# Kernel optimization log

Hardware: AMD Instinct MI355X
Metric: run time of the kernel (lower is better)

The kernel has to match this reference:

```python
import jax, jax.numpy as jnp
import numpy as np
from jax import lax

B, L, DM = 1, 2048, 1024   # batch, seq len, d_model
N = 16                     # d_state
K = 4                      # d_conv
DI = 2 * DM                # d_inner = d_model * expand_factor


def silu(v):
    return v * jax.nn.sigmoid(v)


def setup_inputs() -> dict:
    key = jax.random.key(0)
    ks = jax.random.split(key, 11)
    s = 0.02
    f32 = jnp.float32
    return {
        "x": jax.random.normal(ks[0], (B, L, DM), f32),
        "W_in": jax.random.normal(ks[1], (2 * DI, DM), f32) * s,
        "b_in": jnp.zeros((2 * DI,), f32),
        "W_conv": jax.random.normal(ks[2], (DI, 1, K), f32) * s,  # depthwise conv kernel (torch layout)
        "b_conv": jnp.zeros((DI,), f32),
        "W_x": jax.random.normal(ks[3], (DI + 2 * N, DI), f32) * s,
        "b_x": jnp.zeros((DI + 2 * N,), f32),
        "W_out": jax.random.normal(ks[4], (DM, DI), f32) * s,
        "b_out": jnp.zeros((DM,), f32),
        "A_log": jax.random.normal(ks[5], (DI, N), f32),
        "D": jnp.ones((DI,), f32),
    }


def reference(x, W_in, b_in, W_conv, b_conv, W_x, b_x, W_out, b_out, A_log, D):
    Bsz = x.shape[0]
    # in_proj and split into ssm branch / residual gate branch
    xr = x @ W_in.T + b_in                      # (B, L, 2*DI)
    xi, res = jnp.split(xr, 2, axis=-1)
    # causal depthwise conv1d: torch pads (K-1) both sides then slices [:L] == left-pad K-1
    xc = jnp.transpose(xi, (0, 2, 1))           # (B, DI, L)
    xc = lax.conv_general_dilated(
        xc, W_conv, window_strides=(1,), padding=[(K - 1, 0)],
        dimension_numbers=("NCH", "OIH", "NCH"), feature_group_count=DI,
    ) + b_conv[None, :, None]
    xi = silu(jnp.transpose(xc, (0, 2, 1)))     # (B, L, DI)
    # selective-scan parameterization
    proj = xi @ W_x.T + b_x                      # (B, L, DI + 2N)
    delta = jax.nn.softplus(proj[..., :DI])      # (B, L, DI)
    B_ssm = proj[..., DI:DI + N]                 # (B, L, N)
    C_ssm = proj[..., DI + N:]                   # (B, L, N)
    A = -jnp.exp(A_log)                          # (DI, N)
    dA = jnp.exp(delta[..., None] * A)                               # (B, L, DI, N)
    dBx = delta[..., None] * B_ssm[:, :, None, :] * xi[..., None]    # (B, L, DI, N)

    def step(h, inp):
        da, dbx, c = inp
        h = da * h + dbx                         # (B, DI, N)
        y = jnp.einsum("bdn,bn->bd", h, c)
        return h, y

    h0 = jnp.zeros((Bsz, DI, N), x.dtype)
    _, ys = lax.scan(
        step, h0,
        (jnp.swapaxes(dA, 0, 1), jnp.swapaxes(dBx, 0, 1), jnp.swapaxes(C_ssm, 0, 1)),
    )
    y = jnp.swapaxes(ys, 0, 1) + xi * D          # skip connection
    y = y * silu(res)                            # gate
    return y @ W_out.T + b_out                   # (B, L, DM)
```

## Files before the change

### kernel.cpp

```cpp
#include <hip/hip_runtime.h>
#include <stdint.h>

#define L_SEQ 2048
#define DMODEL 1024
#define DI_DIM 2048
#define NSSM 16
#define NPROJ 2080
#define NCHUNK 64
#define LCHUNK 32
#define NBC 32

typedef __attribute__((ext_vector_type(8))) short bf16x8;
typedef __attribute__((ext_vector_type(8))) unsigned short u16x8;
typedef __attribute__((ext_vector_type(4))) float f32x4;

__device__ __forceinline__ float bf2f(unsigned short u) {
  union { uint32_t u; float f; } v; v.u = (uint32_t)u << 16; return v.f;
}
__device__ __forceinline__ unsigned short f2bf(float f) {
  union { float f; uint32_t u; } v; v.f = f;
  uint32_t u = v.u;
  return (unsigned short)((u + 0x7fffu + ((u >> 16) & 1u)) >> 16);
}
__device__ __forceinline__ void async16(const void* g, void* l) {
  __builtin_amdgcn_global_load_lds(
      (__attribute__((address_space(1))) void*)(g),
      (__attribute__((address_space(3))) void*)(l), 16, 0, 0);
}
__device__ __forceinline__ float softplusf(float p) {
  return (p > 20.f) ? p : __logf(1.f + __expf(p));
}
__device__ __forceinline__ float siluf(float x) {
  return x * __builtin_amdgcn_rcpf(1.f + __expf(-x));
}

#define WAITV(N) asm volatile("s_waitcnt vmcnt(" #N ")" ::: "memory")
#define GBAR()                                   \
  {                                              \
    __builtin_amdgcn_s_barrier();                \
    asm volatile("" ::: "memory");               \
  }

#define CVT_N1 524288
#define CVT_N2 (CVT_N1 + 1048576)
#define CVT_N3 (CVT_N2 + 1064960)
#define CVT_N4 (CVT_N3 + 524288)
__global__ void k_convert4(const float* __restrict__ x, const float* __restrict__ win,
                           const float* __restrict__ wx, const float* __restrict__ wout,
                           unsigned short* __restrict__ xb, unsigned short* __restrict__ winb,
                           unsigned short* __restrict__ wxb, unsigned short* __restrict__ woutb,
                           unsigned short* __restrict__ wbct) {
  int i = blockIdx.x * 256 + threadIdx.x;
  const float4* src; unsigned short* dst; int j;
  bool isWx = false;
  if (i < CVT_N1)      { src = (const float4*)x;    dst = xb;    j = i; }
  else if (i < CVT_N2) { src = (const float4*)win;  dst = winb;  j = i - CVT_N1; }
  else if (i < CVT_N3) { src = (const float4*)wx;   dst = wxb;   j = i - CVT_N2; isWx = true; }
  else if (i < CVT_N4) { src = (const float4*)wout; dst = woutb; j = i - CVT_N3; }
  else return;
  float4 v = src[j];
  ushort4 o;
  o.x = f2bf(v.x); o.y = f2bf(v.y); o.z = f2bf(v.z); o.w = f2bf(v.w);
  ((ushort4*)dst)[j] = o;
  if (isWx) {
    int r = j >> 9;
    if (r >= DI_DIM) {
      int n = r - DI_DIM;
      int d4 = (j & 511) * 4;
      unsigned short ov[4] = {o.x, o.y, o.z, o.w};
#pragma unroll
      for (int k = 0; k < 4; k++) {
        int d = d4 + k;
        wbct[((size_t)(d >> 3) * NBC + n) * 8 + (d & 7)] = ov[k];
      }
    }
  }
}

__global__ void k_wout_cvt(const float* __restrict__ in, unsigned short* __restrict__ out) {
  int i = blockIdx.x * 256 + threadIdx.x;
  float4 v = ((const float4*)in)[i];
  ushort4 o;
  o.x = f2bf(v.x); o.y = f2bf(v.y); o.z = f2bf(v.z); o.w = f2bf(v.w);
  ((ushort4*)out)[i] = o;
}


#define GSTAGE(BUF, KT)                                                        \
  {                                                                            \
    async16(ap + (KT), &As[BUF][soA]);                                         \
    async16(bp0 + (KT), &Bs[BUF][soB0]);                                       \
    async16(bp1 + (KT), &Bs[BUF][soB1]);                                       \
  }

#define GCOMPUTE(BUF)                                                          \
  {                                                                            \
    bf16x8 af[4], bfv[2];                                                      \
    _Pragma("unroll")                                                          \
    for (int i = 0; i < 4; i++)                                                \
      af[i] = *(const bf16x8*)&As[BUF][i * 512 + ro];                          \
    _Pragma("unroll")                                                          \
    for (int j = 0; j < 2; j++)                                                \
      bfv[j] = *(const bf16x8*)&Bs[BUF][(wave * 2 + j) * 512 + ro];            \
    _Pragma("unroll")                                                          \
    for (int i = 0; i < 4; i++)                                                \
      _Pragma("unroll")                                                        \
      for (int j = 0; j < 2; j++)                                              \
        acc[i][j] = __builtin_amdgcn_mfma_f32_16x16x32_bf16(af[i], bfv[j],     \
                                                        acc[i][j], 0, 0, 0);   \
  }

#define DEFINE_GEMM_BT(NAME, OutT)                                             \
__global__ __launch_bounds__(256) void NAME(                                   \
    const unsigned short* __restrict__ A, const unsigned short* __restrict__ B,\
    const float* __restrict__ bias, OutT* __restrict__ C,                      \
    int M, int N, int K, int ldc) {                                            \
  __shared__ unsigned short As[3][64 * 32];                                    \
  __shared__ unsigned short Bs[3][128 * 32];                                   \
  const int tid = threadIdx.x;                                                 \
  const int wave = tid >> 6;                                                   \
  const int lane = tid & 63;                                                   \
  const int m0 = blockIdx.x * 64;       \
  const int n0 = blockIdx.y * 128;                                             \
  const int kLen = K / gridDim.z;                                              \
  const int kLo = blockIdx.z * kLen;                                           \
  const int srow = lane >> 2;                                                  \
  const int scol = ((lane & 3) ^ ((lane >> 3) & 3)) * 8;                       \
  int ar = m0 + wave * 16 + srow;         if (ar > M - 1) ar = M - 1;          \
  int br0 = n0 + wave * 32 + srow;        if (br0 > N - 1) br0 = N - 1;        \
  int br1 = n0 + wave * 32 + 16 + srow;   if (br1 > N - 1) br1 = N - 1;        \
  const unsigned short* ap  = A + (size_t)ar * K + scol + kLo;                 \
  const unsigned short* bp0 = B + (size_t)br0 * K + scol + kLo;                \
  const unsigned short* bp1 = B + (size_t)br1 * K + scol + kLo;                \
  const int soA  = wave * 512;                                                 \
  const int soB0 = (wave * 2) * 512;                                           \
  const int soB1 = (wave * 2 + 1) * 512;                                       \
  const int mrow = lane & 15;                                                  \
  const int swz8 = (((lane >> 4) ^ ((mrow >> 1) & 3)) * 8);                    \
  const int ro = mrow * 32 + swz8;                                             \
  f32x4 acc[4][2];                                                             \
  _Pragma("unroll")                                                            \
  for (int i = 0; i < 4; i++)                                                  \
    _Pragma("unroll")                                                          \
    for (int j = 0; j < 2; j++) acc[i][j] = (f32x4){0.f, 0.f, 0.f, 0.f};       \
  const int niter = kLen / 32;                                                 \
  _Pragma("unroll")                                                            \
  for (int j = 0; j < 2; j++) GSTAGE(j, j * 32)                                \
  int cur = 0, nxt = 2;                                                        \
  for (int t = 0; t < niter - 2; t++) {                                        \
    WAITV(3);                                                                  \
    GBAR()                                                                     \
    GSTAGE(nxt, (t + 2) * 32)                                                  \
    GCOMPUTE(cur)                                                              \
    cur = (cur == 2) ? 0 : cur + 1;                                            \
    nxt = (nxt == 2) ? 0 : nxt + 1;                                            \
  }                                                                            \
  WAITV(3); GBAR()                                                             \
  GCOMPUTE(cur) cur = (cur == 2) ? 0 : cur + 1;                                \
  WAITV(0); GBAR()                                                             \
  GCOMPUTE(cur)                                                                \
  const bool withBias = (gridDim.z == 1);                                      \
  OutT* Cz = C + (size_t)blockIdx.z * ((size_t)M * ldc);                       \
  _Pragma("unroll")                                                            \
  for (int j = 0; j < 2; j++) {                                                \
    int col = n0 + wave * 32 + j * 16 + (lane & 15);                           \
    if (col < N) {                                                             \
      float bv = withBias ? bias[col] : 0.f;                                   \
      _Pragma("unroll")                                                        \
      for (int i = 0; i < 4; i++) {                                            \
        int rbase = m0 + i * 16 + (lane >> 4) * 4;                             \
        _Pragma("unroll")                                                      \
        for (int r = 0; r < 4; r++) {                                          \
          float v = acc[i][j][r] + bv;                                         \
          if constexpr (sizeof(OutT) == 2)                                     \
            Cz[(size_t)(rbase + r) * ldc + col] = (OutT)f2bf(v);               \
          else                                                                 \
            Cz[(size_t)(rbase + r) * ldc + col] = (OutT)v;                     \
        }                                                                      \
      }                                                                        \
    }                                                                          \
  }                                                                            \
}

DEFINE_GEMM_BT(k_gemm_xr, unsigned short)
DEFINE_GEMM_BT(k_gemm_proj, float)
DEFINE_GEMM_BT(k_gemm_out, float)

__global__ void k_reduce_out(const float* __restrict__ part, const float* __restrict__ bias,
                             float* __restrict__ out) {
  int i = blockIdx.x * 256 + threadIdx.x;
  float4 a = ((const float4*)part)[i];
  float4 b = ((const float4*)(part + (size_t)L_SEQ * DMODEL))[i];
  int col = (i * 4) & (DMODEL - 1);
  float4 bb = *(const float4*)&bias[col];
  float4 o;
  o.x = a.x + b.x + bb.x; o.y = a.y + b.y + bb.y;
  o.z = a.z + b.z + bb.z; o.w = a.w + b.w + bb.w;
  ((float4*)out)[i] = o;
}

#define TCONV 8
__global__ __launch_bounds__(256) void k_conv_silu_bc(
    const unsigned short* __restrict__ xr, const float* __restrict__ Wc,
    const float* __restrict__ bc, const unsigned short* __restrict__ wbct,
    const float* __restrict__ bx, unsigned short* __restrict__ xcb,
    float* __restrict__ proj) {
  __shared__ float xi_sh[TCONV][DI_DIM];
  __shared__ float red[8][TCONV][NBC];
  const int tid = threadIdx.x;
  const int t0 = blockIdx.x * TCONV;
  const int d8 = tid * 8;
  float wd[8][4], bb[8];
#pragma unroll
  for (int j = 0; j < 8; j++) {
    float4 w = *(const float4*)&Wc[(size_t)(d8 + j) * 4];
    wd[j][0] = w.x; wd[j][1] = w.y; wd[j][2] = w.z; wd[j][3] = w.w;
  }
  {
    float4 b0 = *(const float4*)&bc[d8];
    float4 b1 = *(const float4*)&bc[d8 + 4];
    bb[0] = b0.x; bb[1] = b0.y; bb[2] = b0.z; bb[3] = b0.w;
    bb[4] = b1.x; bb[5] = b1.y; bb[6] = b1.z; bb[7] = b1.w;
  }
  const size_t rs = 2 * DI_DIM;
  u16x8 xw0 = (u16x8)(unsigned short)0, xw1 = xw0, xw2 = xw0;
  if (t0 >= 3) xw0 = *(const u16x8*)&xr[(size_t)(t0 - 3) * rs + d8];
  if (t0 >= 2) xw1 = *(const u16x8*)&xr[(size_t)(t0 - 2) * rs + d8];
  if (t0 >= 1) xw2 = *(const u16x8*)&xr[(size_t)(t0 - 1) * rs + d8];
  for (int t = 0; t < TCONV; t++) {
    u16x8 xw3 = *(const u16x8*)&xr[(size_t)(t0 + t) * rs + d8];
    u16x8 o;
#pragma unroll
    for (int j = 0; j < 8; j++) {
      float acc = bb[j] + bf2f(xw0[j]) * wd[j][0] + bf2f(xw1[j]) * wd[j][1] +
                  bf2f(xw2[j]) * wd[j][2] + bf2f(xw3[j]) * wd[j][3];
      unsigned short ob = f2bf(siluf(acc));
      o[j] = ob;
      xi_sh[t][d8 + j] = bf2f(ob);
    }
    *(u16x8*)&xcb[(size_t)(t0 + t) * DI_DIM + d8] = o;
    xw0 = xw1; xw1 = xw2; xw2 = xw3;
  }
  __syncthreads();
  const int n = tid & 31, seg = tid >> 5;
  float acc[TCONV];
#pragma unroll
  for (int t = 0; t < TCONV; t++) acc[t] = 0.f;
  for (int c = 0; c < 32; c++) {
    int dc = seg * 32 + c;
    u16x8 w8 = *(const u16x8*)&wbct[((size_t)dc * NBC + n) * 8];
    float wf[8];
#pragma unroll
    for (int j = 0; j < 8; j++) wf[j] = bf2f(w8[j]);
#pragma unroll
    for (int t = 0; t < TCONV; t++) {
      const f32x4* xp = (const f32x4*)&xi_sh[t][dc * 8];
      f32x4 x0 = xp[0], x1 = xp[1];
      acc[t] += x0[0] * wf[0] + x0[1] * wf[1] + x0[2] * wf[2] + x0[3] * wf[3] +
                x1[0] * wf[4] + x1[1] * wf[5] + x1[2] * wf[6] + x1[3] * wf[7];
    }
  }
#pragma unroll
  for (int t = 0; t < TCONV; t++) red[seg][t][n] = acc[t];
  __syncthreads();
  {
    int t = tid >> 5, nn = tid & 31;
    float s = 0.f;
#pragma unroll
    for (int w = 0; w < 8; w++) s += red[w][t][nn];
    s += bx[DI_DIM + nn];
    proj[(size_t)(t0 + t) * NPROJ + DI_DIM + nn] = s;
  }
}

__global__ __launch_bounds__(256) void k_scan_a(
    const float* __restrict__ proj, const unsigned short* __restrict__ xcb,
    const float* __restrict__ A_log,
    float* __restrict__ Sdelta, float* __restrict__ hstate) {
  __shared__ float Bsh[LCHUNK * NSSM];
  const int d = blockIdx.x * 256 + threadIdx.x;
  const int c = blockIdx.y;
  const int t0 = c * LCHUNK;
  for (int i = threadIdx.x; i < LCHUNK * NSSM; i += 256) {
    int t = i >> 4, n = i & 15;
    Bsh[i] = proj[(size_t)(t0 + t) * NPROJ + DI_DIM + n];
  }
  __syncthreads();
  float Ar[NSSM], h[NSSM];
#pragma unroll
  for (int n = 0; n < NSSM; n++) {
    Ar[n] = -__expf(A_log[d * NSSM + n]);
    h[n] = 0.f;
  }
  const float* pp = proj + (size_t)t0 * NPROJ + d;
  const unsigned short* xp = xcb + (size_t)t0 * DI_DIM + d;
  float p_nxt = pp[0];
  unsigned short x_nxt = xp[0];
  float sd = 0.f;
  for (int t = 0; t < LCHUNK; t++) {
    float p = p_nxt;
    unsigned short xu = x_nxt;
    if (t + 1 < LCHUNK) {
      p_nxt = pp[(size_t)(t + 1) * NPROJ];
      x_nxt = xp[(size_t)(t + 1) * DI_DIM];
    }
    float delta = softplusf(p);
    float dx = delta * bf2f(xu);
    sd += delta;
#pragma unroll
    for (int n = 0; n < NSSM; n++)
      h[n] = __expf(delta * Ar[n]) * h[n] + dx * Bsh[t * NSSM + n];
  }
  Sdelta[(size_t)c * DI_DIM + d] = sd;
  float4* hp = (float4*)&hstate[((size_t)c * DI_DIM + d) * NSSM];
  hp[0] = (float4){h[0], h[1], h[2], h[3]};
  hp[1] = (float4){h[4], h[5], h[6], h[7]};
  hp[2] = (float4){h[8], h[9], h[10], h[11]};
  hp[3] = (float4){h[12], h[13], h[14], h[15]};
}

__global__ void k_scan_b(const float* __restrict__ A_log,
                         const float* __restrict__ Sdelta,
                         float* __restrict__ hstate) {
  int tid = blockIdx.x * 256 + threadIdx.x;
  int d = tid >> 4;
  float A = -__expf(A_log[tid]);
  float carry = 0.f;
  for (int cb = 0; cb < NCHUNK; cb += 8) {
    float v[8], s[8];
#pragma unroll
    for (int j = 0; j < 8; j++) {
      v[j] = hstate[(size_t)(cb + j) * DI_DIM * NSSM + tid];
      s[j] = Sdelta[(size_t)(cb + j) * DI_DIM + d];
    }
#pragma unroll
    for (int j = 0; j < 8; j++) {
      hstate[(size_t)(cb + j) * DI_DIM * NSSM + tid] = carry;
      carry = __expf(A * s[j]) * carry + v[j];
    }
  }
}

__global__ __launch_bounds__(256) void k_scan_c(
    const float* __restrict__ proj, const unsigned short* __restrict__ xcb,
    const float* __restrict__ A_log, const float* __restrict__ h0,
    const float* __restrict__ Dvec, const unsigned short* __restrict__ xr,
    unsigned short* __restrict__ ybf) {
  __shared__ float Bsh[LCHUNK * NSSM];
  __shared__ float Csh[LCHUNK * NSSM];
  const int d = blockIdx.x * 256 + threadIdx.x;
  const int c = blockIdx.y;
  const int t0 = c * LCHUNK;
  for (int i = threadIdx.x; i < LCHUNK * NSSM; i += 256) {
    int t = i >> 4, n = i & 15;
    size_t ob = (size_t)(t0 + t) * NPROJ + DI_DIM + n;
    Bsh[i] = proj[ob];
    Csh[i] = proj[ob + NSSM];
  }
  __syncthreads();
  float Ar[NSSM], h[NSSM];
#pragma unroll
  for (int n = 0; n < NSSM; n++)
    Ar[n] = -__expf(A_log[d * NSSM + n]);
  const float4* h0p = (const float4*)&h0[((size_t)c * DI_DIM + d) * NSSM];
  float4 hv0 = h0p[0], hv1 = h0p[1], hv2 = h0p[2], hv3 = h0p[3];
  h[0] = hv0.x; h[1] = hv0.y; h[2] = hv0.z; h[3] = hv0.w;
  h[4] = hv1.x; h[5] = hv1.y; h[6] = hv1.z; h[7] = hv1.w;
  h[8] = hv2.x; h[9] = hv2.y; h[10] = hv2.z; h[11] = hv2.w;
  h[12] = hv3.x; h[13] = hv3.y; h[14] = hv3.z; h[15] = hv3.w;
  float Dd = Dvec[d];
  const float* pp = proj + (size_t)t0 * NPROJ + d;
  const unsigned short* xp = xcb + (size_t)t0 * DI_DIM + d;
  const unsigned short* rp = xr + (size_t)t0 * (2 * DI_DIM) + DI_DIM + d;
  float p_nxt = pp[0];
  unsigned short x_nxt = xp[0];
  unsigned short r_nxt = rp[0];
  for (int t = 0; t < LCHUNK; t++) {
    float p = p_nxt;
    unsigned short xu = x_nxt, ru = r_nxt;
    if (t + 1 < LCHUNK) {
      p_nxt = pp[(size_t)(t + 1) * NPROJ];
      x_nxt = xp[(size_t)(t + 1) * DI_DIM];
      r_nxt = rp[(size_t)(t + 1) * (2 * DI_DIM)];
    }
    float delta = softplusf(p);
    float xi = bf2f(xu);
    float dx = delta * xi;
    float y = 0.f;
#pragma unroll
    for (int n = 0; n < NSSM; n++) {
      h[n] = __expf(delta * Ar[n]) * h[n] + dx * Bsh[t * NSSM + n];
      y += h[n] * Csh[t * NSSM + n];
    }
    y += xi * Dd;
    y *= siluf(bf2f(ru));
    ybf[(size_t)(t0 + t) * DI_DIM + d] = f2bf(y);
  }
}

extern "C" void kernel_launch(void* const* d_in, const int* in_sizes, int n_in,
                              void* d_out, int out_size, void* d_ws, size_t ws_size,
                              hipStream_t stream) {
  const float* x      = (const float*)d_in[0];
  const float* W_in   = (const float*)d_in[1];
  const float* b_in   = (const float*)d_in[2];
  const float* W_conv = (const float*)d_in[3];
  const float* b_conv = (const float*)d_in[4];
  const float* W_x    = (const float*)d_in[5];
  const float* b_x    = (const float*)d_in[6];
  const float* W_out  = (const float*)d_in[7];
  const float* b_out  = (const float*)d_in[8];
  const float* A_log  = (const float*)d_in[9];
  const float* Dv     = (const float*)d_in[10];
  float* out = (float*)d_out;

  char* ws = (char*)d_ws;
  size_t off = 0;
  auto alloc = [&](size_t bytes) { void* p = ws + off; off += (bytes + 255) & ~(size_t)255; return p; };
  unsigned short* win_bf = (unsigned short*)alloc((size_t)4096 * DMODEL * 2);
  unsigned short* wx_bf  = (unsigned short*)alloc((size_t)NPROJ * DI_DIM * 2);
  unsigned short* x_bf   = (unsigned short*)alloc((size_t)L_SEQ * DMODEL * 2);
  unsigned short* xr_bf  = (unsigned short*)alloc((size_t)L_SEQ * 2 * DI_DIM * 2);
  unsigned short* xcb    = (unsigned short*)alloc((size_t)L_SEQ * DI_DIM * 2);
  float* proj            = (float*)alloc((size_t)L_SEQ * NPROJ * 4);
  float* Sdelta          = (float*)alloc((size_t)NCHUNK * DI_DIM * 4);
  float* hstate          = (float*)alloc((size_t)NCHUNK * DI_DIM * NSSM * 4);
  unsigned short* wbct   = (unsigned short*)alloc((size_t)DI_DIM * NBC * 2);
  if (off > ws_size) return;
  unsigned short* ybf     = win_bf;
  unsigned short* wout_bf = x_bf;
  float* part             = proj;

  unsigned short* wout2 = nullptr;
  {
    size_t need = (size_t)DMODEL * DI_DIM * 2;
    if (off + need <= ws_size) wout2 = (unsigned short*)alloc(need);
  }
  if (wout2) {
    k_convert4<<<CVT_N4 / 256, 256, 0, stream>>>(x, W_in, W_x, W_out,
                                                 x_bf, win_bf, wx_bf, wout2, wbct);
    wout_bf = wout2;
  } else {
    k_convert4<<<CVT_N3 / 256, 256, 0, stream>>>(x, W_in, W_x, W_out,
                                                 x_bf, win_bf, wx_bf, x_bf , wbct);
  }

  {
    dim3 g(L_SEQ / 64, 4096 / 128);
    k_gemm_xr<<<g, 256, 0, stream>>>(x_bf, win_bf, b_in, xr_bf, L_SEQ, 4096, DMODEL, 4096);
  }
  if (!wout2) {
    k_wout_cvt<<<(DMODEL * DI_DIM / 4) / 256, 256, 0, stream>>>(W_out, wout_bf);
  }
  k_conv_silu_bc<<<L_SEQ / TCONV, 256, 0, stream>>>(xr_bf, W_conv, b_conv, wbct,
                                                    b_x, xcb, proj);
  {
    dim3 g(L_SEQ / 64, 2048 / 128);
    k_gemm_proj<<<g, 256, 0, stream>>>(xcb, wx_bf, b_x, proj, L_SEQ, 2048, DI_DIM, NPROJ);
  }
  {
    dim3 ga(DI_DIM / 256, NCHUNK);
    k_scan_a<<<ga, 256, 0, stream>>>(proj, xcb, A_log, Sdelta, hstate);
    k_scan_b<<<(DI_DIM * NSSM) / 256, 256, 0, stream>>>(A_log, Sdelta, hstate);
    k_scan_c<<<ga, 256, 0, stream>>>(proj, xcb, A_log, hstate, Dv, xr_bf, ybf);
  }
  {
    dim3 g(L_SEQ / 64, DMODEL / 128, 2);
    k_gemm_out<<<g, 256, 0, stream>>>(ybf, wout_bf, b_out, part, L_SEQ, DMODEL, DI_DIM, DMODEL);
    k_reduce_out<<<(L_SEQ * DMODEL / 4) / 256, 256, 0, stream>>>(part, b_out, out);
  }
}
```

Measured before the change: 264.4 us.

## Fuse three scan phases into one cooperative kernel; drop out-GEMM split-K

Replaces the three chunked selective-scan kernels with a single cooperative kernel that uses grid-wide syncs between the per-chunk local scan, the cross-chunk carry propagation and the final output pass, keeping A and the B/C tiles in registers and shared memory across phases. This removes two kernel launches and recomputation of setup. The output GEMM no longer splits K across two partial buffers, which removes the separate reduction kernel and its extra memory traffic but halves the grid parallelism of that GEMM. Grid syncs over 512 blocks need all of them co-resident and add barrier cost, and the carry phase uses only a subset of blocks.

```diff
diff --git a/kernel.cpp b/kernel.cpp
--- a/kernel.cpp
+++ b/kernel.cpp
@@ -1,5 +1,8 @@
 #include <hip/hip_runtime.h>
+#include <hip/hip_cooperative_groups.h>
 #include <stdint.h>
+
+namespace cg = cooperative_groups;
 
 #define L_SEQ 2048
 #define DMODEL 1024
@@ -186,19 +189,6 @@
 DEFINE_GEMM_BT(k_gemm_proj, float)
 DEFINE_GEMM_BT(k_gemm_out, float)
 
-__global__ void k_reduce_out(const float* __restrict__ part, const float* __restrict__ bias,
-                             float* __restrict__ out) {
-  int i = blockIdx.x * 256 + threadIdx.x;
-  float4 a = ((const float4*)part)[i];
-  float4 b = ((const float4*)(part + (size_t)L_SEQ * DMODEL))[i];
-  int col = (i * 4) & (DMODEL - 1);
-  float4 bb = *(const float4*)&bias[col];
-  float4 o;
-  o.x = a.x + b.x + bb.x; o.y = a.y + b.y + bb.y;
-  o.z = a.z + b.z + bb.z; o.w = a.w + b.w + bb.w;
-  ((float4*)out)[i] = o;
-}
-
 #define TCONV 8
 __global__ __launch_bounds__(256) void k_conv_silu_bc(
     const unsigned short* __restrict__ xr, const float* __restrict__ Wc,
@@ -270,6 +260,117 @@
     for (int w = 0; w < 8; w++) s += red[w][t][nn];
     s += bx[DI_DIM + nn];
     proj[(size_t)(t0 + t) * NPROJ + DI_DIM + nn] = s;
+  }
+}
+
+__global__ __launch_bounds__(256) void k_scan_fused(
+    const float* __restrict__ proj, const unsigned short* __restrict__ xcb,
+    const float* __restrict__ A_log, float* __restrict__ Sdelta,
+    float* __restrict__ hstate, const float* __restrict__ Dvec,
+    const unsigned short* __restrict__ xr, unsigned short* __restrict__ ybf) {
+  cg::grid_group grid = cg::this_grid();
+  __shared__ float Bsh[LCHUNK * NSSM];
+  __shared__ float Csh[LCHUNK * NSSM];
+  const int d = blockIdx.x * 256 + threadIdx.x;
+  const int c = blockIdx.y;
+  const int t0 = c * LCHUNK;
+  for (int i = threadIdx.x; i < LCHUNK * NSSM; i += 256) {
+    int t = i >> 4, n = i & 15;
+    size_t ob = (size_t)(t0 + t) * NPROJ + DI_DIM + n;
+    Bsh[i] = proj[ob];
+    Csh[i] = proj[ob + NSSM];
+  }
+  __syncthreads();
+  float Ar[NSSM], h[NSSM];
+#pragma unroll
+  for (int n = 0; n < NSSM; n++) {
+    Ar[n] = -__expf(A_log[d * NSSM + n]);
+    h[n] = 0.f;
+  }
+  const float* pp = proj + (size_t)t0 * NPROJ + d;
+  const unsigned short* xp = xcb + (size_t)t0 * DI_DIM + d;
+  {
+    float p_nxt = pp[0];
+    unsigned short x_nxt = xp[0];
+    float sd = 0.f;
+    for (int t = 0; t < LCHUNK; t++) {
+      float p = p_nxt;
+      unsigned short xu = x_nxt;
+      if (t + 1 < LCHUNK) {
+        p_nxt = pp[(size_t)(t + 1) * NPROJ];
+        x_nxt = xp[(size_t)(t + 1) * DI_DIM];
+      }
+      float delta = softplusf(p);
+      float dx = delta * bf2f(xu);
+      sd += delta;
+#pragma unroll
+      for (int n = 0; n < NSSM; n++)
+        h[n] = __expf(delta * Ar[n]) * h[n] + dx * Bsh[t * NSSM + n];
+    }
+    Sdelta[(size_t)c * DI_DIM + d] = sd;
+    float4* hp = (float4*)&hstate[((size_t)c * DI_DIM + d) * NSSM];
+    hp[0] = (float4){h[0], h[1], h[2], h[3]};
+    hp[1] = (float4){h[4], h[5], h[6], h[7]};
+    hp[2] = (float4){h[8], h[9], h[10], h[11]};
+    hp[3] = (float4){h[12], h[13], h[14], h[15]};
+  }
+  grid.sync();
+  {
+    int flat = blockIdx.y * gridDim.x + blockIdx.x;
+    if (flat < (DI_DIM * NSSM) / 256) {
+      int tid = flat * 256 + threadIdx.x;
+      int dd = tid >> 4;
+      float A = -__expf(A_log[tid]);
+      float carry = 0.f;
+      for (int cb = 0; cb < NCHUNK; cb += 8) {
+        float v[8], s[8];
+#pragma unroll
+        for (int j = 0; j < 8; j++) {
+          v[j] = hstate[(size_t)(cb + j) * DI_DIM * NSSM + tid];
+          s[j] = Sdelta[(size_t)(cb + j) * DI_DIM + dd];
+        }
+#pragma unroll
+        for (int j = 0; j < 8; j++) {
+          hstate[(size_t)(cb + j) * DI_DIM * NSSM + tid] = carry;
+          carry = __expf(A * s[j]) * carry + v[j];
+        }
+      }
+    }
+  }
+  grid.sync();
+  {
+    const float4* h0p = (const float4*)&hstate[((size_t)c * DI_DIM + d) * NSSM];
+    float4 hv0 = h0p[0], hv1 = h0p[1], hv2 = h0p[2], hv3 = h0p[3];
+    h[0] = hv0.x; h[1] = hv0.y; h[2] = hv0.z; h[3] = hv0.w;
+    h[4] = hv1.x; h[5] = hv1.y; h[6] = hv1.z; h[7] = hv1.w;
+    h[8] = hv2.x; h[9] = hv2.y; h[10] = hv2.z; h[11] = hv2.w;
+    h[12] = hv3.x; h[13] = hv3.y; h[14] = hv3.z; h[15] = hv3.w;
+    float Dd = Dvec[d];
+    const unsigned short* rp = xr + (size_t)t0 * (2 * DI_DIM) + DI_DIM + d;
+    float p_nxt = pp[0];
+    unsigned short x_nxt = xp[0];
+    unsigned short r_nxt = rp[0];
+    for (int t = 0; t < LCHUNK; t++) {
+      float p = p_nxt;
+      unsigned short xu = x_nxt, ru = r_nxt;
+      if (t + 1 < LCHUNK) {
+        p_nxt = pp[(size_t)(t + 1) * NPROJ];
+        x_nxt = xp[(size_t)(t + 1) * DI_DIM];
+        r_nxt = rp[(size_t)(t + 1) * (2 * DI_DIM)];
+      }
+      float delta = softplusf(p);
+      float xi = bf2f(xu);
+      float dx = delta * xi;
+      float y = 0.f;
+#pragma unroll
+      for (int n = 0; n < NSSM; n++) {
+        h[n] = __expf(delta * Ar[n]) * h[n] + dx * Bsh[t * NSSM + n];
+        y += h[n] * Csh[t * NSSM + n];
+      }
+      y += xi * Dd;
+      y *= siluf(bf2f(ru));
+      ybf[(size_t)(t0 + t) * DI_DIM + d] = f2bf(y);
+    }
   }
 }
 
@@ -429,7 +530,6 @@
   if (off > ws_size) return;
   unsigned short* ybf     = win_bf;
   unsigned short* wout_bf = x_bf;
-  float* part             = proj;
 
   unsigned short* wout2 = nullptr;
   {
@@ -459,14 +559,29 @@
     k_gemm_proj<<<g, 256, 0, stream>>>(xcb, wx_bf, b_x, proj, L_SEQ, 2048, DI_DIM, NPROJ);
   }
   {
-    dim3 ga(DI_DIM / 256, NCHUNK);
-    k_scan_a<<<ga, 256, 0, stream>>>(proj, xcb, A_log, Sdelta, hstate);
-    k_scan_b<<<(DI_DIM * NSSM) / 256, 256, 0, stream>>>(A_log, Sdelta, hstate);
-    k_scan_c<<<ga, 256, 0, stream>>>(proj, xcb, A_log, hstate, Dv, xr_bf, ybf);
-  }
-  {
-    dim3 g(L_SEQ / 64, DMODEL / 128, 2);
-    k_gemm_out<<<g, 256, 0, stream>>>(ybf, wout_bf, b_out, part, L_SEQ, DMODEL, DI_DIM, DMODEL);
-    k_reduce_out<<<(L_SEQ * DMODEL / 4) / 256, 256, 0, stream>>>(part, b_out, out);
-  }
-}
+    static int coopOK = -1;
+    if (coopOK < 0) {
+      int v = 0;
+      hipError_t e = hipDeviceGetAttribute(&v, hipDeviceAttributeCooperativeLaunch, 0);
+      coopOK = (e == hipSuccess && v) ? 1 : 0;
+    }
+    if (coopOK) {
+      const float* projc = proj;
+      const unsigned short* xcbc = xcb;
+      const unsigned short* xrc = xr_bf;
+      void* args[] = {(void*)&projc, (void*)&xcbc, (void*)&A_log, (void*)&Sdelta,
+                      (void*)&hstate, (void*)&Dv, (void*)&xrc, (void*)&ybf};
+      hipLaunchCooperativeKernel((const void*)k_scan_fused, dim3(DI_DIM / 256, NCHUNK),
+                                 dim3(256), args, 0, stream);
+    } else {
+      dim3 ga(DI_DIM / 256, NCHUNK);
+      k_scan_a<<<ga, 256, 0, stream>>>(proj, xcb, A_log, Sdelta, hstate);
+      k_scan_b<<<(DI_DIM * NSSM) / 256, 256, 0, stream>>>(A_log, Sdelta, hstate);
+      k_scan_c<<<ga, 256, 0, stream>>>(proj, xcb, A_log, hstate, Dv, xr_bf, ybf);
+    }
+  }
+  {
+    dim3 g(L_SEQ / 64, DMODEL / 128);
+    k_gemm_out<<<g, 256, 0, stream>>>(ybf, wout_bf, b_out, out, L_SEQ, DMODEL, DI_DIM, DMODEL);
+  }
+}
```

New measurement: 430.8 us. 63.0% more time.
